# Performance work log

Measured on AMD Instinct MI355X. Metric: run time of the kernel, lower is better.

Reference implementation:

```python
import jax, jax.numpy as jnp
import numpy as np

B, C, H, W_SP, OC, K = 16, 64, 128, 128, 128, 3
SPARSITY = 0.9


def setup_inputs() -> dict:
    key = jax.random.key(0)
    kx, kmask, ksign = jax.random.split(key, 3)
    x = jax.random.normal(kx, (B, C, H, W_SP), dtype=jnp.float32)
    n = OC * C * K * K
    signs = jax.random.bernoulli(ksign, 0.5, (n,)).astype(jnp.float32) * 2.0 - 1.0
    mask = jax.random.bernoulli(kmask, SPARSITY, (n,)).astype(jnp.float32)
    # Original: weight.view((OC, C*K*K)).t() -> (CK, OC) layout used against im2col columns.
    weight = (signs * mask).reshape(OC, C * K * K).T  # (CK, OC)
    return {"x": x, "weight": weight}


def reference(x, weight):
    # Intended math of RandomBinaryConvV1: cols = unfold(x) (B, CK, L);
    # out[b, l, oc] = sum_k cols[b, k, l] * weight[k, oc]  (ternary weight),
    # i.e. a standard 2D convolution with a ternary kernel, 'same' padding, stride 1.
    b, c, h, w = x.shape
    ck, oc = weight.shape
    k = int(round(np.sqrt(ck // c)))  # static shapes -> Python int
    kern = weight.T.reshape(oc, c, k, k)  # OIHW
    pad = k // 2
    out = jax.lax.conv_general_dilated(
        x, kern,
        window_strides=(1, 1),
        padding=[(pad, pad), (pad, pad)],
        dimension_numbers=("NCHW", "OIHW", "NCHW"),
    )
    return out  # (B, OC, H, W)
```

## Files before the change

### kernel.cpp

```cpp
#include <hip/hip_runtime.h>
#include <hip/hip_bf16.h>
#include <cstdint>

#define Cc 64
#define Hh 128
#define Ww 128
#define OCn 128
#define HBLK 4
#define WT 64
#define WLs 72
#define HP 130
#define WP 136
#define NT 18
#define SLOT_SHORTS (WLs * Cc)
#define XP_BYTES (((size_t)16 * HP * WP * Cc) * 2)
#define PRE_BLOCKS (16 * HP)

typedef float f32x4 __attribute__((ext_vector_type(4)));
typedef __bf16 bf16x8 __attribute__((ext_vector_type(8)));
typedef short s16x8 __attribute__((ext_vector_type(8)));

union bs8 { s16x8 s; bf16x8 b; };
__device__ __forceinline__ bf16x8 as_bf16x8(s16x8 s) { bs8 u; u.s = s; return u.b; }

__global__ __launch_bounds__(256) void prepass_kernel(const float* __restrict__ x,
                                                      const float* __restrict__ w,
                                                      unsigned short* __restrict__ xp,
                                                      s16x8* __restrict__ wpf) {
  int bid = blockIdx.x;
  int t = threadIdx.x;
  if (bid >= PRE_BLOCKS) {
    int idx = (bid - PRE_BLOCKS) * 256 + t;
    int l = idx & 63;
    int mb = (idx >> 6) & 7;
    int tt = idx >> 9;
    int ch = tt & 1;
    int o = tt >> 1;
    int kh = o / 3, kw = o % 3;
    int oc = mb * 16 + (l & 15);
    int kl0 = (l >> 4) * 8;
    bf16x8 v;
#pragma unroll
    for (int j = 0; j < 8; ++j) {
      int c = ch * 32 + kl0 + j;
      int ko = (c * 3 + kh) * 3 + kw;
      v[j] = (__bf16)w[ko * OCn + oc];
    }
    bs8 u; u.b = v;
    wpf[idx] = u.s;
    return;
  }
  int u = (bid >> 3) + (bid & 7) * 260;
  int b = u / 130, hp = u - b * 130;
  size_t obase = ((size_t)b * HP + hp) * WP * Cc;
  s16x8 z = (s16x8){0, 0, 0, 0, 0, 0, 0, 0};
  if (hp == 0 || hp == HP - 1) {
    for (int ck = t; ck < WP * Cc / 8; ck += 256)
      *(s16x8*)(xp + obase + (size_t)ck * 8) = z;
    return;
  }
  int h = hp - 1;
  __shared__ float tile[Cc][Ww + 1];
  int wpx = t & 127, chalf = t >> 7;
#pragma unroll
  for (int k = 0; k < 32; ++k) {
    int c = chalf * 32 + k;
    tile[c][wpx] = __builtin_nontemporal_load(
        &x[(((size_t)b * Cc + c) * Hh + h) * Ww + wpx]);
  }
  __syncthreads();
#pragma unroll
  for (int k = 0; k < 4; ++k) {
    int idx = k * 256 + t;
    int ww = idx >> 3, cg = idx & 7;
    bf16x8 v;
#pragma unroll
    for (int j = 0; j < 8; ++j) v[j] = (__bf16)tile[cg * 8 + j][ww];
    bs8 uu; uu.b = v;
    *(s16x8*)(xp + obase + (size_t)(ww + 1) * Cc + cg * 8) = uu.s;
  }
  if (t < 16) {
    int wz = (t >> 3) ? (Ww + 1) : 0;
    *(s16x8*)(xp + obase + (size_t)wz * Cc + (t & 7) * 8) = z;
  }
}

__global__ __launch_bounds__(256) void conv_mfma_kernel(
    const unsigned short* __restrict__ xp, const s16x8* __restrict__ wpf,
    float* __restrict__ out) {
  __shared__ __align__(16) short xt[4 * SLOT_SHORTS];
  int tid = threadIdx.x;
  int bid = blockIdx.x;
  int wk = (bid >> 3) + (bid & 7) * 128;
  int wt = wk & 1;
  int hb = (wk >> 1) & 31;
  int b = wk >> 6;
  int h0 = hb * HBLK;
  int wv = tid >> 6, lane = tid & 63;
  int l15 = lane & 15, l4 = lane >> 4;

  auto stage = [&](int h_img) {
    int slot = (h_img + 1) & 3;
    size_t rbase = (((size_t)b * HP + (h_img + 1)) * WP + wt * WT) * Cc;
    int cg = lane & 7, wo = lane >> 3;
    const unsigned short* src0 = xp + rbase + (size_t)wo * Cc + ((cg ^ wo) << 3);
    for (int i = wv; i < 9; i += 4) {
      const unsigned short* src = src0 + (size_t)i * 8 * Cc;
      short* dst = &xt[slot * SLOT_SHORTS + i * 512];
      __builtin_amdgcn_global_load_lds(
          (const __attribute__((address_space(1))) void*)src,
          (__attribute__((address_space(3))) void*)dst, 16, 0, 0);
    }
  };

  stage(h0 - 1);
  stage(h0);
  stage(h0 + 1);

  for (int i = 0; i < HBLK; ++i) {
    int h = h0 + i;
    __syncthreads();
    if (i < HBLK - 1) stage(h + 2);

    f32x4 acc[2][4];
#pragma unroll
    for (int mi = 0; mi < 2; ++mi)
#pragma unroll
      for (int ni = 0; ni < 4; ++ni)
        acc[mi][ni] = (f32x4){0.f, 0.f, 0.f, 0.f};

#pragma unroll
    for (int t = 0; t < NT; ++t) {
      int kh = t / 6, kw = (t >> 1) % 3, ch = t & 1;
      bf16x8 a0 = as_bf16x8(wpf[(t * 8 + wv * 2 + 0) * 64 + lane]);
      bf16x8 a1 = as_bf16x8(wpf[(t * 8 + wv * 2 + 1) * 64 + lane]);
      int slot = (h + kh) & 3;
      int cgr = ch * 4 + l4;
#pragma unroll
      for (int ni = 0; ni < 4; ++ni) {
        int wl2 = ni * 16 + l15 + kw;
        int caddr = slot * SLOT_SHORTS + wl2 * Cc + ((cgr ^ (wl2 & 7)) << 3);
        bf16x8 bfr = as_bf16x8(*(const s16x8*)&xt[caddr]);
        acc[0][ni] = __builtin_amdgcn_mfma_f32_16x16x32_bf16(a0, bfr, acc[0][ni], 0, 0, 0);
        acc[1][ni] = __builtin_amdgcn_mfma_f32_16x16x32_bf16(a1, bfr, acc[1][ni], 0, 0, 0);
      }
    }

#pragma unroll
    for (int mi = 0; mi < 2; ++mi)
#pragma unroll
      for (int ni = 0; ni < 4; ++ni) {
        int oc = wv * 32 + mi * 16 + l4 * 4;
        int w_img = wt * WT + ni * 16 + l15;
        float* po = out + (((size_t)(b * OCn + oc)) * Hh + h) * Ww + w_img;
#pragma unroll
        for (int r = 0; r < 4; ++r)
          __builtin_nontemporal_store(acc[mi][ni][r], po + (size_t)r * Hh * Ww);
      }
  }
}

extern "C" void kernel_launch(void* const* d_in, const int* in_sizes, int n_in,
                              void* d_out, int out_size, void* d_ws, size_t ws_size,
                              hipStream_t stream) {
  const float* x = (const float*)d_in[0];
  const float* w = (const float*)d_in[1];
  float* out = (float*)d_out;
  unsigned short* xp = (unsigned short*)d_ws;
  s16x8* wpf = (s16x8*)((char*)d_ws + XP_BYTES);
  prepass_kernel<<<PRE_BLOCKS + 36, 256, 0, stream>>>(x, w, xp, wpf);
  conv_mfma_kernel<<<1024, 256, 0, stream>>>(xp, (const s16x8*)wpf, out);
}
```

Baseline: 62.28 us.

## Widen conv tile to full row and keep weight fragments in registers

The conv kernel now processes a full 128-wide image row per block instead of two 64-wide halves, halving the grid to 512 blocks and doubling the MFMA N-tiles per wave. All 18x2 weight fragments are loaded into registers once per block instead of being re-read from global memory for every output row. The prepass also switches its input reads to vectorized float4 loads. The costs are higher register pressure (36 bf16x8 fragments plus 16 accumulators), a larger LDS footprint of roughly 70 KB, and fewer blocks available for latency hiding.

```diff
diff --git a/kernel.cpp b/kernel.cpp
--- a/kernel.cpp
+++ b/kernel.cpp
@@ -7,12 +7,11 @@
 #define Ww 128
 #define OCn 128
 #define HBLK 4
-#define WT 64
-#define WLs 72
+#define WPS 136
 #define HP 130
 #define WP 136
 #define NT 18
-#define SLOT_SHORTS (WLs * Cc)
+#define SLOT_SHORTS (WPS * Cc)
 #define XP_BYTES (((size_t)16 * HP * WP * Cc) * 2)
 #define PRE_BLOCKS (16 * HP)
 
@@ -61,12 +60,13 @@
   }
   int h = hp - 1;
   __shared__ float tile[Cc][Ww + 1];
-  int wpx = t & 127, chalf = t >> 7;
+  int w4 = (t & 31) * 4, c0 = (t >> 5) * 8;
 #pragma unroll
-  for (int k = 0; k < 32; ++k) {
-    int c = chalf * 32 + k;
-    tile[c][wpx] = __builtin_nontemporal_load(
-        &x[(((size_t)b * Cc + c) * Hh + h) * Ww + wpx]);
+  for (int k = 0; k < 8; ++k) {
+    int c = c0 + k;
+    f32x4 v = *(const f32x4*)&x[(((size_t)b * Cc + c) * Hh + h) * Ww + w4];
+#pragma unroll
+    for (int j = 0; j < 4; ++j) tile[c][w4 + j] = v[j];
   }
   __syncthreads();
 #pragma unroll
@@ -85,26 +85,32 @@
   }
 }
 
-__global__ __launch_bounds__(256) void conv_mfma_kernel(
+__global__ __launch_bounds__(256, 2) void conv_mfma_kernel(
     const unsigned short* __restrict__ xp, const s16x8* __restrict__ wpf,
     float* __restrict__ out) {
   __shared__ __align__(16) short xt[4 * SLOT_SHORTS];
   int tid = threadIdx.x;
   int bid = blockIdx.x;
-  int wk = (bid >> 3) + (bid & 7) * 128;
-  int wt = wk & 1;
-  int hb = (wk >> 1) & 31;
-  int b = wk >> 6;
+  int wk = (bid >> 3) + (bid & 7) * 64;
+  int hb = wk & 31;
+  int b = wk >> 5;
   int h0 = hb * HBLK;
   int wv = tid >> 6, lane = tid & 63;
   int l15 = lane & 15, l4 = lane >> 4;
 
+  bf16x8 af[NT][2];
+#pragma unroll
+  for (int t = 0; t < NT; ++t)
+#pragma unroll
+    for (int mi = 0; mi < 2; ++mi)
+      af[t][mi] = as_bf16x8(wpf[(t * 8 + wv * 2 + mi) * 64 + lane]);
+
   auto stage = [&](int h_img) {
     int slot = (h_img + 1) & 3;
-    size_t rbase = (((size_t)b * HP + (h_img + 1)) * WP + wt * WT) * Cc;
+    size_t rbase = ((size_t)b * HP + (h_img + 1)) * WP * Cc;
     int cg = lane & 7, wo = lane >> 3;
     const unsigned short* src0 = xp + rbase + (size_t)wo * Cc + ((cg ^ wo) << 3);
-    for (int i = wv; i < 9; i += 4) {
+    for (int i = wv; i < 17; i += 4) {
       const unsigned short* src = src0 + (size_t)i * 8 * Cc;
       short* dst = &xt[slot * SLOT_SHORTS + i * 512];
       __builtin_amdgcn_global_load_lds(
@@ -122,36 +128,34 @@
     __syncthreads();
     if (i < HBLK - 1) stage(h + 2);
 
-    f32x4 acc[2][4];
+    f32x4 acc[2][8];
 #pragma unroll
     for (int mi = 0; mi < 2; ++mi)
 #pragma unroll
-      for (int ni = 0; ni < 4; ++ni)
+      for (int ni = 0; ni < 8; ++ni)
         acc[mi][ni] = (f32x4){0.f, 0.f, 0.f, 0.f};
 
 #pragma unroll
     for (int t = 0; t < NT; ++t) {
       int kh = t / 6, kw = (t >> 1) % 3, ch = t & 1;
-      bf16x8 a0 = as_bf16x8(wpf[(t * 8 + wv * 2 + 0) * 64 + lane]);
-      bf16x8 a1 = as_bf16x8(wpf[(t * 8 + wv * 2 + 1) * 64 + lane]);
       int slot = (h + kh) & 3;
       int cgr = ch * 4 + l4;
 #pragma unroll
-      for (int ni = 0; ni < 4; ++ni) {
+      for (int ni = 0; ni < 8; ++ni) {
         int wl2 = ni * 16 + l15 + kw;
         int caddr = slot * SLOT_SHORTS + wl2 * Cc + ((cgr ^ (wl2 & 7)) << 3);
         bf16x8 bfr = as_bf16x8(*(const s16x8*)&xt[caddr]);
-        acc[0][ni] = __builtin_amdgcn_mfma_f32_16x16x32_bf16(a0, bfr, acc[0][ni], 0, 0, 0);
-        acc[1][ni] = __builtin_amdgcn_mfma_f32_16x16x32_bf16(a1, bfr, acc[1][ni], 0, 0, 0);
+        acc[0][ni] = __builtin_amdgcn_mfma_f32_16x16x32_bf16(af[t][0], bfr, acc[0][ni], 0, 0, 0);
+        acc[1][ni] = __builtin_amdgcn_mfma_f32_16x16x32_bf16(af[t][1], bfr, acc[1][ni], 0, 0, 0);
       }
     }
 
 #pragma unroll
     for (int mi = 0; mi < 2; ++mi)
 #pragma unroll
-      for (int ni = 0; ni < 4; ++ni) {
+      for (int ni = 0; ni < 8; ++ni) {
         int oc = wv * 32 + mi * 16 + l4 * 4;
-        int w_img = wt * WT + ni * 16 + l15;
+        int w_img = ni * 16 + l15;
         float* po = out + (((size_t)(b * OCn + oc)) * Hh + h) * Ww + w_img;
 #pragma unroll
         for (int r = 0; r < 4; ++r)
@@ -169,5 +173,5 @@
   unsigned short* xp = (unsigned short*)d_ws;
   s16x8* wpf = (s16x8*)((char*)d_ws + XP_BYTES);
   prepass_kernel<<<PRE_BLOCKS + 36, 256, 0, stream>>>(x, w, xp, wpf);
-  conv_mfma_kernel<<<1024, 256, 0, stream>>>(xp, (const s16x8*)wpf, out);
+  conv_mfma_kernel<<<512, 256, 0, stream>>>(xp, (const s16x8*)wpf, out);
 }
```

Result: slower. 65.87 us (+5.8%).
